# Optimization experiments

Hardware: AMD Instinct MI355X
Metric: run time of the kernel (lower is better)

Reference implementation:

```python
import jax, jax.numpy as jnp
import numpy as np

B, T, D, H = 4, 2048, 1024, 16
DH = D // H          # 64
HALF = DH // 2       # 32


def _rope_tables(T, half, base=10000.0):
    inv_freq = 1.0 / (base ** (np.arange(half, dtype=np.float32) / half))
    t = np.arange(T, dtype=np.float32)
    ang = np.outer(t, inv_freq)                       # [T, half]
    cos = jnp.asarray(np.cos(ang))[None, None]        # [1,1,T,half]
    sin = jnp.asarray(np.sin(ang))[None, None]
    return cos, sin


def setup_inputs() -> dict:
    key = jax.random.key(0)
    kx, kq, kp = jax.random.split(key, 3)
    cos, sin = _rope_tables(T, HALF)
    return {
        "x": jax.random.normal(kx, (B, T, D), dtype=jnp.float32),
        "cos": cos,
        "sin": sin,
        "W_qkv": jax.random.normal(kq, (3 * D, D), dtype=jnp.float32) * (D ** -0.5),
        "W_proj": jax.random.normal(kp, (D, D), dtype=jnp.float32) * (D ** -0.5),
    }


def _apply_rope(q, k, cos, sin):
    # q,k: [B,H,T,dh]; cos,sin: [1,1,T,dh/2]
    t = q.shape[2]
    c, s = cos[:, :, :t, :], sin[:, :, :t, :]
    h = q.shape[-1] // 2
    q1, q2 = q[..., :h], q[..., h:]
    k1, k2 = k[..., :h], k[..., h:]
    q_rot = jnp.concatenate([q1 * c - q2 * s, q1 * s + q2 * c], axis=-1)
    k_rot = jnp.concatenate([k1 * c - k2 * s, k1 * s + k2 * c], axis=-1)
    return q_rot, k_rot


def reference(x, cos, sin, W_qkv, W_proj):
    Bb, Tt, C = x.shape
    qkv = x @ W_qkv.T                                 # [B,T,3C]
    q, k, v = jnp.split(qkv, 3, axis=2)
    # [B,T,C] -> [B,H,T,dh]
    q = q.reshape(Bb, Tt, H, DH).transpose(0, 2, 1, 3)
    k = k.reshape(Bb, Tt, H, DH).transpose(0, 2, 1, 3)
    v = v.reshape(Bb, Tt, H, DH).transpose(0, 2, 1, 3)
    q, k = _apply_rope(q, k, cos, sin)
    w = jnp.einsum("bhqd,bhkd->bhqk", q, k) * (DH ** -0.5)
    causal = jnp.tril(jnp.ones((Tt, Tt), dtype=bool))
    w = jnp.where(causal, w, -jnp.inf)
    w = jax.nn.softmax(w.astype(jnp.float32), axis=-1).astype(x.dtype)
    out = jnp.einsum("bhqk,bhkd->bhqd", w, v)
    # XSA: subtract self-value contribution (diagonal attention weight)
    self_w = jnp.diagonal(w, axis1=-2, axis2=-1)[..., None]  # [B,H,T,1]
    out = out - self_w * v
    out = out.transpose(0, 2, 1, 3).reshape(Bb, Tt, C)
    return out @ W_proj.T
```

## Files before the change

kernel.cpp:

```cpp
#include <hip/hip_runtime.h>

constexpr int Tq = 2048;
constexpr int Dq = 1024;

typedef __bf16 bf16x8 __attribute__((ext_vector_type(8)));
typedef float f32x4 __attribute__((ext_vector_type(4)));
typedef _Float16 f16;
typedef f16 f16x4 __attribute__((ext_vector_type(4)));
typedef unsigned short u16;
typedef u16 u16x4 __attribute__((ext_vector_type(4)));
typedef u16 u16x8 __attribute__((ext_vector_type(8)));

__device__ __forceinline__ u16 f2bf(float f) {
    unsigned int u = __float_as_uint(f);
    u += 0x7fffu + ((u >> 16) & 1u);
    return (u16)(u >> 16);
}

__device__ __forceinline__ void gld_lds16(const void* g, void* l) {
    __builtin_amdgcn_global_load_lds(
        (const __attribute__((address_space(1))) unsigned int*)g,
        (__attribute__((address_space(3))) unsigned int*)l, 16, 0, 0);
}

__global__ void cvt3_f32_bf16(const float* __restrict__ a, u16* __restrict__ oa, int na,
                              const float* __restrict__ b, u16* __restrict__ ob, int nb,
                              const float* __restrict__ c, u16* __restrict__ oc, int nc) {
    int i = blockIdx.x * 256 + threadIdx.x;
    const float* in; u16* out;
    if (i < na) { in = a; out = oa; }
    else if (i < na + nb) { in = b; out = ob; i -= na; }
    else if (i < na + nb + nc) { in = c; out = oc; i -= na + nb; }
    else return;
    float4 v = ((const float4*)in)[i];
    u16x4 o;
    o.x = f2bf(v.x); o.y = f2bf(v.y); o.z = f2bf(v.z); o.w = f2bf(v.w);
    ((u16x4*)out)[i] = o;
}

__global__ __launch_bounds__(512, 2) void gemm_qkv(const u16* __restrict__ A,
                                                   const u16* __restrict__ B,
                                                   const float* __restrict__ cosT,
                                                   const float* __restrict__ sinT,
                                                   u16* __restrict__ Qb,
                                                   u16* __restrict__ Kb,
                                                   f16* __restrict__ Vtg) {
    constexpr int K = 1024, nk = K / 64;
    __shared__ __align__(16) u16 smem[65536];
    const int t = threadIdx.x;
    const int lane = t & 63;
    const int wave = t >> 6;
    const int l16 = lane & 15;
    const int quad = lane >> 4;
    const int wr = wave >> 2;
    const int wc = wave & 3;
    const int bm = blockIdx.x * 256;
    const int by = blockIdx.y;
    const int bn = by * 256;

    const int srow = t >> 3;
    const int sgc = (t & 7) ^ (srow & 7);
    const u16* Ab = A + (size_t)(bm + srow) * K + sgc * 8;
    const u16* Bb = B + (size_t)(bn + srow) * K + sgc * 8;

    f32x4 acc[8][4] = {};

    auto stageA = [&](int kt, int q) {
        gld_lds16(Ab + (size_t)q * 64 * K + kt * 64,
                  (char*)smem + (kt & 1) * 65536 + q * 8192 + t * 16);
    };
    auto stageB = [&](int kt, int q) {
        gld_lds16(Bb + (size_t)q * 64 * K + kt * 64,
                  (char*)smem + (kt & 1) * 65536 + 32768 + q * 8192 + t * 16);
    };

    stageB(0, 0); stageB(0, 1); stageB(0, 2); stageB(0, 3);
    stageA(0, 0); stageA(0, 2); stageA(0, 1); stageA(0, 3);

    const int cc0 = quad ^ (l16 & 7);
    const int cc1 = (4 + quad) ^ (l16 & 7);

    for (int kt = 0; kt < nk; kt++) {
        const u16* As = smem + (kt & 1) * 32768;
        const u16* Bs = As + 16384;
        const bool pre = (kt + 1 < nk);

        asm volatile("s_waitcnt vmcnt(2)\n\ts_barrier" ::: "memory");

        bf16x8 af[4], bf[4];
        if (pre) { stageB(kt + 1, 0); stageB(kt + 1, 1); }
#pragma unroll
        for (int m = 0; m < 4; m++)
            af[m] = *(const bf16x8*)&As[(wr * 128 + m * 16 + l16) * 64 + cc0 * 8];
#pragma unroll
        for (int n = 0; n < 4; n++)
            bf[n] = *(const bf16x8*)&Bs[(wc * 64 + n * 16 + l16) * 64 + cc0 * 8];
        __builtin_amdgcn_s_setprio(1);
#pragma unroll
        for (int m = 0; m < 4; m++)
#pragma unroll
            for (int n = 0; n < 4; n++)
                acc[m][n] = __builtin_amdgcn_mfma_f32_16x16x32_bf16(af[m], bf[n], acc[m][n], 0, 0, 0);
        __builtin_amdgcn_s_setprio(0);

        if (pre) asm volatile("s_waitcnt vmcnt(2)\n\ts_barrier" ::: "memory");
        else     asm volatile("s_waitcnt vmcnt(0)\n\ts_barrier" ::: "memory");

        if (pre) { stageB(kt + 1, 2); stageB(kt + 1, 3); }
#pragma unroll
        for (int m = 0; m < 4; m++)
            af[m] = *(const bf16x8*)&As[(wr * 128 + (m + 4) * 16 + l16) * 64 + cc0 * 8];
        __builtin_amdgcn_s_setprio(1);
#pragma unroll
        for (int m = 0; m < 4; m++)
#pragma unroll
            for (int n = 0; n < 4; n++)
                acc[m + 4][n] = __builtin_amdgcn_mfma_f32_16x16x32_bf16(af[m], bf[n], acc[m + 4][n], 0, 0, 0);
        __builtin_amdgcn_s_setprio(0);

        if (pre) { stageA(kt + 1, 0); stageA(kt + 1, 2); }
#pragma unroll
        for (int m = 0; m < 4; m++)
            af[m] = *(const bf16x8*)&As[(wr * 128 + m * 16 + l16) * 64 + cc1 * 8];
#pragma unroll
        for (int n = 0; n < 4; n++)
            bf[n] = *(const bf16x8*)&Bs[(wc * 64 + n * 16 + l16) * 64 + cc1 * 8];
        __builtin_amdgcn_s_setprio(1);
#pragma unroll
        for (int m = 0; m < 4; m++)
#pragma unroll
            for (int n = 0; n < 4; n++)
                acc[m][n] = __builtin_amdgcn_mfma_f32_16x16x32_bf16(af[m], bf[n], acc[m][n], 0, 0, 0);
        __builtin_amdgcn_s_setprio(0);

        if (pre) { stageA(kt + 1, 1); stageA(kt + 1, 3); }
#pragma unroll
        for (int m = 0; m < 4; m++)
            af[m] = *(const bf16x8*)&As[(wr * 128 + (m + 4) * 16 + l16) * 64 + cc1 * 8];
        __builtin_amdgcn_s_setprio(1);
#pragma unroll
        for (int m = 0; m < 4; m++)
#pragma unroll
            for (int n = 0; n < 4; n++)
                acc[m + 4][n] = __builtin_amdgcn_mfma_f32_16x16x32_bf16(af[m], bf[n], acc[m + 4][n], 0, 0, 0);
        __builtin_amdgcn_s_setprio(0);
    }

    const int kind = by >> 2;
    if (kind < 2) {
        u16* Out = kind ? Kb : Qb;
        const float qscale = kind ? 1.f : 0.18033688011112042f;
        const int h = ((by & 3) << 2) + wc;
#pragma unroll
        for (int m = 0; m < 8; m++)
#pragma unroll
            for (int r = 0; r < 4; r++) {
                const int gm = bm + wr * 128 + m * 16 + quad * 4 + r;
                const int b = gm >> 11, tt = gm & 2047;
                const size_t row = ((size_t)(b * 16 + h) * Tq + tt) * 64;
#pragma unroll
                for (int jj = 0; jj < 2; jj++) {
                    const int dd = jj * 16 + l16;
                    const float c = cosT[tt * 32 + dd];
                    const float s = sinT[tt * 32 + dd];
                    const float v1 = acc[m][jj][r];
                    const float v2 = acc[m][jj + 2][r];
                    Out[row + dd]      = f2bf((v1 * c - v2 * s) * qscale);
                    Out[row + dd + 32] = f2bf((v1 * s + v2 * c) * qscale);
                }
            }
    } else {
        const int h = ((by & 3) << 2) + wc;
#pragma unroll
        for (int m = 0; m < 8; m++) {
            const int gm0 = bm + wr * 128 + m * 16 + quad * 4;
            const int b = gm0 >> 11, tt = gm0 & 2047;
#pragma unroll
            for (int n = 0; n < 4; n++) {
                const int d = n * 16 + l16;
                f16x4 o = {(f16)acc[m][n][0], (f16)acc[m][n][1],
                           (f16)acc[m][n][2], (f16)acc[m][n][3]};
                *(f16x4*)&Vtg[((size_t)(b * 16 + h) * 64 + d) * Tq + tt] = o;
            }
        }
    }
}

__global__ __launch_bounds__(256) void gemm_bt(const u16* __restrict__ A,
                                               const u16* __restrict__ B,
                                               float* __restrict__ Cv,
                                               int M, int N, int K) {
    __shared__ u16 As[128 * 32];
    __shared__ u16 Bs[128 * 32];
    const int t = threadIdx.x;
    const int lane = t & 63;
    const int wave = t >> 6;
    const int l16 = lane & 15;
    const int quad = lane >> 4;
    const int bm = blockIdx.x * 128;
    const int bn = blockIdx.y * 128;
    const int wm = (wave & 1) * 64;
    const int wn = (wave >> 1) * 64;
    const int srow = t >> 2;
    const int scol = (t & 3) * 8;

    f32x4 acc[4][4] = {};

    const u16* Ab = A + (size_t)(bm + srow) * K + scol;
    const u16* Bb = B + (size_t)(bn + srow) * K + scol;

    for (int k0 = 0; k0 < K; k0 += 32) {
        gld_lds16(Ab + k0,                    (char*)As + t * 16);
        gld_lds16(Ab + (size_t)64 * K + k0,   (char*)As + 4096 + t * 16);
        gld_lds16(Bb + k0,                    (char*)Bs + t * 16);
        gld_lds16(Bb + (size_t)64 * K + k0,   (char*)Bs + 4096 + t * 16);
        __syncthreads();

        bf16x8 af[4], bf[4];
#pragma unroll
        for (int i = 0; i < 4; i++) {
            af[i] = *(const bf16x8*)&As[(wm + i * 16 + l16) * 32 + quad * 8];
            bf[i] = *(const bf16x8*)&Bs[(wn + i * 16 + l16) * 32 + quad * 8];
        }
#pragma unroll
        for (int i = 0; i < 4; i++)
#pragma unroll
            for (int j = 0; j < 4; j++)
                acc[i][j] = __builtin_amdgcn_mfma_f32_16x16x32_bf16(af[i], bf[j], acc[i][j], 0, 0, 0);
        __syncthreads();
    }

#pragma unroll
    for (int i = 0; i < 4; i++)
#pragma unroll
        for (int j = 0; j < 4; j++)
#pragma unroll
            for (int r = 0; r < 4; r++) {
                const int gm = bm + wm + i * 16 + quad * 4 + r;
                const int gn = bn + wn + j * 16 + l16;
                Cv[(size_t)gm * N + gn] = acc[i][j][r];
            }
}

template <bool MASK>
__device__ __forceinline__ void flash_tile(const u16* __restrict__ Ks,
                                           const f16* __restrict__ Vs,
                                           const bf16x8& qf0, const bf16x8& qf1,
                                           int l16, int quad, int i_loc,
                                           float& l_run, f32x4* o_acc) {
    f32x4 s[4];
    const int cp0 = quad ^ (l16 & 7);
    const int cp1 = (4 + quad) ^ (l16 & 7);
    __builtin_amdgcn_s_setprio(1);
#pragma unroll
    for (int tn = 0; tn < 4; tn++) {
        const int jrow = tn * 16 + l16;
        bf16x8 kf0 = *(const bf16x8*)&Ks[jrow * 64 + cp0 * 8];
        bf16x8 kf1 = *(const bf16x8*)&Ks[jrow * 64 + cp1 * 8];
        f32x4 z = {0.f, 0.f, 0.f, 0.f};
        z = __builtin_amdgcn_mfma_f32_16x16x32_bf16(kf0, qf0, z, 0, 0, 0);
        z = __builtin_amdgcn_mfma_f32_16x16x32_bf16(kf1, qf1, z, 0, 0, 0);
        s[tn] = z;
    }
    __builtin_amdgcn_s_setprio(0);
    float rsa[4];
#pragma unroll
    for (int tn = 0; tn < 4; tn++) {
        float rs = 0.f;
#pragma unroll
        for (int r = 0; r < 4; r++) {
            float v = s[tn][r];
            if (MASK) {
                const int j_loc = tn * 16 + quad * 4 + r;
                if (j_loc > i_loc) v = -1e30f;
            }
            float p = exp2f(v);
            rs += p;
            if (MASK) {
                const int j_loc = tn * 16 + quad * 4 + r;
                if (j_loc == i_loc) p = 0.f;
            }
            s[tn][r] = p;
        }
        rsa[tn] = rs;
    }
    l_run += (rsa[0] + rsa[1]) + (rsa[2] + rsa[3]);

    f16x4 pf[4];
#pragma unroll
    for (int tk = 0; tk < 4; tk++)
        pf[tk] = f16x4{(f16)s[tk][0], (f16)s[tk][1], (f16)s[tk][2], (f16)s[tk][3]};
    __builtin_amdgcn_s_setprio(1);
#pragma unroll
    for (int td = 0; td < 4; td++) {
        const int drow = td * 16 + l16;
#pragma unroll
        for (int tk = 0; tk < 4; tk++) {
            const int cp = (2 * tk + (quad >> 1)) ^ (l16 & 7);
            f16x4 vf = *(const f16x4*)&Vs[drow * 64 + cp * 8 + (quad & 1) * 4];
            o_acc[td] = __builtin_amdgcn_mfma_f32_16x16x16f16(vf, pf[tk], o_acc[td], 0, 0, 0);
        }
    }
    __builtin_amdgcn_s_setprio(0);
}

__global__ __launch_bounds__(512, 4) void flash(const u16* __restrict__ Qb,
                                                const u16* __restrict__ Kb,
                                                const f16* __restrict__ Vtg,
                                                u16* __restrict__ Ob) {
    __shared__ __align__(16) char smem[65536];

    const int t = threadIdx.x, lane = t & 63, wave = t >> 6;
    const int l16 = lane & 15, quad = lane >> 4;
    const int i = blockIdx.x;
    const int xcd = i & 7, w = i >> 3;
    const int bh = xcd * 8 + (w >> 4);
    const int b = bh >> 4, h = bh & 15;
    const int x = w & 15;
    const int qt = (wave < 4) ? x : (31 - x);
    const int q0w = qt * 64;
    const u16* Qp = Qb + (size_t)bh * Tq * 64;
    const u16* Kp = Kb + (size_t)bh * Tq * 64;
    const f16* Vp = Vtg + (size_t)bh * 64 * Tq;

    const int i_abs = q0w + (wave & 3) * 16 + l16;
    bf16x8 qf0 = *(const bf16x8*)(Qp + (size_t)i_abs * 64 + quad * 8);
    bf16x8 qf1 = *(const bf16x8*)(Qp + (size_t)i_abs * 64 + 32 + quad * 8);
    asm volatile("s_waitcnt vmcnt(0)" : "+v"(qf0), "+v"(qf1) :: "memory");

    float l_run = 0.f;
    f32x4 o_acc[4] = {};

    const int srow = t >> 3;
    const int sc = (t & 7) ^ (srow & 7);
    const int diag_n = qt;
    const int i_tloc = (wave & 3) * 16 + l16;
    const int nt = 32 - x;

    auto stage = [&](int n) {
        const int j0 = n * 64;
        char* buf = smem + (n & 3) * 16384;
        gld_lds16(Kp + (size_t)(j0 + srow) * 64 + sc * 8, buf + t * 16);
        gld_lds16(Vp + (size_t)srow * Tq + j0 + sc * 8,   buf + 8192 + t * 16);
    };

    stage(0);
    stage(1);
    for (int n = 0; n < nt; n++) {
        char* cur = smem + (n & 3) * 16384;
        if (n + 2 < nt) {
            stage(n + 2);
            asm volatile("s_waitcnt vmcnt(4)\n\ts_barrier" ::: "memory");
        } else if (n + 1 < nt) {
            asm volatile("s_waitcnt vmcnt(2)\n\ts_barrier" ::: "memory");
        } else {
            asm volatile("s_waitcnt vmcnt(0)\n\ts_barrier" ::: "memory");
        }
        const u16* Ks = (const u16*)cur;
        const f16* Vs = (const f16*)(cur + 8192);
        if (n < diag_n)
            flash_tile<false>(Ks, Vs, qf0, qf1, l16, quad, i_tloc, l_run, o_acc);
        else if (n == diag_n)
            flash_tile<true>(Ks, Vs, qf0, qf1, l16, quad, i_tloc, l_run, o_acc);
    }

    l_run += __shfl_xor(l_run, 16, 64);
    l_run += __shfl_xor(l_run, 32, 64);
    const float inv_l = 1.f / l_run;

    __syncthreads();
    u16* Os = (u16*)smem;
#pragma unroll
    for (int td = 0; td < 4; td++) {
        u16x4 o;
#pragma unroll
        for (int r = 0; r < 4; r++) o[r] = f2bf(o_acc[td][r] * inv_l);
        *(u16x4*)&Os[wave * 1152 + l16 * 72 + td * 16 + quad * 4] = o;
    }
    __syncthreads();
    const int oi = lane >> 2, od = (lane & 3) * 16;
    u16x8 r0 = *(const u16x8*)&Os[wave * 1152 + oi * 72 + od];
    u16x8 r1 = *(const u16x8*)&Os[wave * 1152 + oi * 72 + od + 8];
    const size_t orow = ((size_t)b * Tq + q0w + (wave & 3) * 16 + oi) * Dq + h * 64 + od;
    *(u16x8*)&Ob[orow] = r0;
    *(u16x8*)&Ob[orow + 8] = r1;
}

extern "C" void kernel_launch(void* const* d_in, const int* in_sizes, int n_in,
                              void* d_out, int out_size, void* d_ws, size_t ws_size,
                              hipStream_t stream) {
    const float* x     = (const float*)d_in[0];
    const float* cosT  = (const float*)d_in[1];
    const float* sinT  = (const float*)d_in[2];
    const float* Wqkv  = (const float*)d_in[3];
    const float* Wproj = (const float*)d_in[4];

    u16* xb     = (u16*)d_ws;
    u16* wqkvb  = xb + (size_t)8192 * 1024;
    u16* wprojb = wqkvb + (size_t)3072 * 1024;
    u16* Qb     = wprojb + (size_t)1024 * 1024;
    u16* Kb     = Qb + (size_t)64 * 2048 * 64;
    f16* Vtg    = (f16*)(Kb + (size_t)64 * 2048 * 64);
    u16* attn   = (u16*)(Vtg + (size_t)64 * 64 * 2048);

    cvt3_f32_bf16<<<12288, 256, 0, stream>>>(x, xb, 2097152,
                                             Wqkv, wqkvb, 786432,
                                             Wproj, wprojb, 262144);

    gemm_qkv<<<dim3(32, 12), 512, 0, stream>>>(xb, wqkvb, cosT, sinT, Qb, Kb, Vtg);
    flash<<<1024, 512, 0, stream>>>(Qb, Kb, Vtg, attn);
    gemm_bt<<<dim3(64, 8), 256, 0, stream>>>(attn, wprojb, (float*)d_out, 8192, 1024, 1024);
}
```

Before: 267.4 us.

## Simplify QKV GEMM to 128x128 single-buffered tiles and double flash K/V staging

Replaces the 256x256 double-buffered, software-pipelined QKV GEMM with a simple 128x128-tile kernel. That kernel loads K-slices of 32 directly to LDS and synchronises twice per iteration, with no prefetch overlap or swizzle. The flash kernel now stages two 64-key tiles per step into a two-slot buffer and waits with vmcnt(0), replacing the 3-deep single-tile ring. This trades latency hiding and data reuse for more blocks and simpler code. It also risks LDS bank conflicts from the removed XOR swizzle in the GEMM.

```diff
diff --git a/kernel.cpp b/kernel.cpp
--- a/kernel.cpp
+++ b/kernel.cpp
@@ -38,124 +38,65 @@
     ((u16x4*)out)[i] = o;
 }
 
-__global__ __launch_bounds__(512, 2) void gemm_qkv(const u16* __restrict__ A,
-                                                   const u16* __restrict__ B,
-                                                   const float* __restrict__ cosT,
-                                                   const float* __restrict__ sinT,
-                                                   u16* __restrict__ Qb,
-                                                   u16* __restrict__ Kb,
-                                                   f16* __restrict__ Vtg) {
-    constexpr int K = 1024, nk = K / 64;
-    __shared__ __align__(16) u16 smem[65536];
+__global__ __launch_bounds__(256) void gemm_qkv(const u16* __restrict__ A,
+                                                const u16* __restrict__ B,
+                                                const float* __restrict__ cosT,
+                                                const float* __restrict__ sinT,
+                                                u16* __restrict__ Qb,
+                                                u16* __restrict__ Kb,
+                                                f16* __restrict__ Vtg) {
+    constexpr int K = 1024, N = 3072;
+    __shared__ u16 As[128 * 32];
+    __shared__ u16 Bs[128 * 32];
     const int t = threadIdx.x;
     const int lane = t & 63;
     const int wave = t >> 6;
     const int l16 = lane & 15;
     const int quad = lane >> 4;
-    const int wr = wave >> 2;
-    const int wc = wave & 3;
-    const int bm = blockIdx.x * 256;
+    const int bm = blockIdx.x * 128;
     const int by = blockIdx.y;
-    const int bn = by * 256;
-
-    const int srow = t >> 3;
-    const int sgc = (t & 7) ^ (srow & 7);
-    const u16* Ab = A + (size_t)(bm + srow) * K + sgc * 8;
-    const u16* Bb = B + (size_t)(bn + srow) * K + sgc * 8;
-
-    f32x4 acc[8][4] = {};
-
-    auto stageA = [&](int kt, int q) {
-        gld_lds16(Ab + (size_t)q * 64 * K + kt * 64,
-                  (char*)smem + (kt & 1) * 65536 + q * 8192 + t * 16);
-    };
-    auto stageB = [&](int kt, int q) {
-        gld_lds16(Bb + (size_t)q * 64 * K + kt * 64,
-                  (char*)smem + (kt & 1) * 65536 + 32768 + q * 8192 + t * 16);
-    };
-
-    stageB(0, 0); stageB(0, 1); stageB(0, 2); stageB(0, 3);
-    stageA(0, 0); stageA(0, 2); stageA(0, 1); stageA(0, 3);
-
-    const int cc0 = quad ^ (l16 & 7);
-    const int cc1 = (4 + quad) ^ (l16 & 7);
-
-    for (int kt = 0; kt < nk; kt++) {
-        const u16* As = smem + (kt & 1) * 32768;
-        const u16* Bs = As + 16384;
-        const bool pre = (kt + 1 < nk);
-
-        asm volatile("s_waitcnt vmcnt(2)\n\ts_barrier" ::: "memory");
+    const int bn = by * 128;
+    const int wm = (wave & 1) * 64;
+    const int wn = (wave >> 1) * 64;
+    const int srow = t >> 2;
+    const int scol = (t & 3) * 8;
+
+    f32x4 acc[4][4] = {};
+
+    const u16* Ab = A + (size_t)(bm + srow) * K + scol;
+    const u16* Bb = B + (size_t)(bn + srow) * K + scol;
+
+    for (int k0 = 0; k0 < K; k0 += 32) {
+        gld_lds16(Ab + k0,                    (char*)As + t * 16);
+        gld_lds16(Ab + (size_t)64 * K + k0,   (char*)As + 4096 + t * 16);
+        gld_lds16(Bb + k0,                    (char*)Bs + t * 16);
+        gld_lds16(Bb + (size_t)64 * K + k0,   (char*)Bs + 4096 + t * 16);
+        __syncthreads();
 
         bf16x8 af[4], bf[4];
-        if (pre) { stageB(kt + 1, 0); stageB(kt + 1, 1); }
-#pragma unroll
-        for (int m = 0; m < 4; m++)
-            af[m] = *(const bf16x8*)&As[(wr * 128 + m * 16 + l16) * 64 + cc0 * 8];
-#pragma unroll
-        for (int n = 0; n < 4; n++)
-            bf[n] = *(const bf16x8*)&Bs[(wc * 64 + n * 16 + l16) * 64 + cc0 * 8];
-        __builtin_amdgcn_s_setprio(1);
-#pragma unroll
-        for (int m = 0; m < 4; m++)
-#pragma unroll
-            for (int n = 0; n < 4; n++)
-                acc[m][n] = __builtin_amdgcn_mfma_f32_16x16x32_bf16(af[m], bf[n], acc[m][n], 0, 0, 0);
-        __builtin_amdgcn_s_setprio(0);
-
-        if (pre) asm volatile("s_waitcnt vmcnt(2)\n\ts_barrier" ::: "memory");
-        else     asm volatile("s_waitcnt vmcnt(0)\n\ts_barrier" ::: "memory");
-
-        if (pre) { stageB(kt + 1, 2); stageB(kt + 1, 3); }
-#pragma unroll
-        for (int m = 0; m < 4; m++)
-            af[m] = *(const bf16x8*)&As[(wr * 128 + (m + 4) * 16 + l16) * 64 + cc0 * 8];
-        __builtin_amdgcn_s_setprio(1);
-#pragma unroll
-        for (int m = 0; m < 4; m++)
-#pragma unroll
-            for (int n = 0; n < 4; n++)
-                acc[m + 4][n] = __builtin_amdgcn_mfma_f32_16x16x32_bf16(af[m], bf[n], acc[m + 4][n], 0, 0, 0);
-        __builtin_amdgcn_s_setprio(0);
-
-        if (pre) { stageA(kt + 1, 0); stageA(kt + 1, 2); }
-#pragma unroll
-        for (int m = 0; m < 4; m++)
-            af[m] = *(const bf16x8*)&As[(wr * 128 + m * 16 + l16) * 64 + cc1 * 8];
-#pragma unroll
-        for (int n = 0; n < 4; n++)
-            bf[n] = *(const bf16x8*)&Bs[(wc * 64 + n * 16 + l16) * 64 + cc1 * 8];
-        __builtin_amdgcn_s_setprio(1);
-#pragma unroll
-        for (int m = 0; m < 4; m++)
-#pragma unroll
-            for (int n = 0; n < 4; n++)
-                acc[m][n] = __builtin_amdgcn_mfma_f32_16x16x32_bf16(af[m], bf[n], acc[m][n], 0, 0, 0);
-        __builtin_amdgcn_s_setprio(0);
-
-        if (pre) { stageA(kt + 1, 1); stageA(kt + 1, 3); }
-#pragma unroll
-        for (int m = 0; m < 4; m++)
-            af[m] = *(const bf16x8*)&As[(wr * 128 + (m + 4) * 16 + l16) * 64 + cc1 * 8];
-        __builtin_amdgcn_s_setprio(1);
-#pragma unroll
-        for (int m = 0; m < 4; m++)
-#pragma unroll
-            for (int n = 0; n < 4; n++)
-                acc[m + 4][n] = __builtin_amdgcn_mfma_f32_16x16x32_bf16(af[m], bf[n], acc[m + 4][n], 0, 0, 0);
-        __builtin_amdgcn_s_setprio(0);
-    }
-
-    const int kind = by >> 2;
+#pragma unroll
+        for (int i = 0; i < 4; i++) {
+            af[i] = *(const bf16x8*)&As[(wm + i * 16 + l16) * 32 + quad * 8];
+            bf[i] = *(const bf16x8*)&Bs[(wn + i * 16 + l16) * 32 + quad * 8];
+        }
+#pragma unroll
+        for (int i = 0; i < 4; i++)
+#pragma unroll
+            for (int j = 0; j < 4; j++)
+                acc[i][j] = __builtin_amdgcn_mfma_f32_16x16x32_bf16(af[i], bf[j], acc[i][j], 0, 0, 0);
+        __syncthreads();
+    }
+
+    const int kind = by >> 3;
     if (kind < 2) {
         u16* Out = kind ? Kb : Qb;
         const float qscale = kind ? 1.f : 0.18033688011112042f;
-        const int h = ((by & 3) << 2) + wc;
-#pragma unroll
-        for (int m = 0; m < 8; m++)
+        const int h = ((by & 7) << 1) + (wn >> 6);
+#pragma unroll
+        for (int i = 0; i < 4; i++)
 #pragma unroll
             for (int r = 0; r < 4; r++) {
-                const int gm = bm + wr * 128 + m * 16 + quad * 4 + r;
+                const int gm = bm + wm + i * 16 + quad * 4 + r;
                 const int b = gm >> 11, tt = gm & 2047;
                 const size_t row = ((size_t)(b * 16 + h) * Tq + tt) * 64;
 #pragma unroll
@@ -163,23 +104,24 @@
                     const int dd = jj * 16 + l16;
                     const float c = cosT[tt * 32 + dd];
                     const float s = sinT[tt * 32 + dd];
-                    const float v1 = acc[m][jj][r];
-                    const float v2 = acc[m][jj + 2][r];
+                    const float v1 = acc[i][jj][r];
+                    const float v2 = acc[i][jj + 2][r];
                     Out[row + dd]      = f2bf((v1 * c - v2 * s) * qscale);
                     Out[row + dd + 32] = f2bf((v1 * s + v2 * c) * qscale);
                 }
             }
     } else {
-        const int h = ((by & 3) << 2) + wc;
-#pragma unroll
-        for (int m = 0; m < 8; m++) {
-            const int gm0 = bm + wr * 128 + m * 16 + quad * 4;
+#pragma unroll
+        for (int i = 0; i < 4; i++) {
+            const int gm0 = bm + wm + i * 16 + quad * 4;
             const int b = gm0 >> 11, tt = gm0 & 2047;
 #pragma unroll
-            for (int n = 0; n < 4; n++) {
-                const int d = n * 16 + l16;
-                f16x4 o = {(f16)acc[m][n][0], (f16)acc[m][n][1],
-                           (f16)acc[m][n][2], (f16)acc[m][n][3]};
+            for (int j = 0; j < 4; j++) {
+                const int col = wn + j * 16 + l16;
+                const int h = ((by & 7) << 1) + (col >> 6);
+                const int d = col & 63;
+                f16x4 o = {(f16)acc[i][j][0], (f16)acc[i][j][1],
+                           (f16)acc[i][j][2], (f16)acc[i][j][3]};
                 *(f16x4*)&Vtg[((size_t)(b * 16 + h) * 64 + d) * Tq + tt] = o;
             }
         }
@@ -336,32 +278,32 @@
     const int diag_n = qt;
     const int i_tloc = (wave & 3) * 16 + l16;
     const int nt = 32 - x;
-
-    auto stage = [&](int n) {
-        const int j0 = n * 64;
-        char* buf = smem + (n & 3) * 16384;
-        gld_lds16(Kp + (size_t)(j0 + srow) * 64 + sc * 8, buf + t * 16);
-        gld_lds16(Vp + (size_t)srow * Tq + j0 + sc * 8,   buf + 8192 + t * 16);
+    const int nt2 = (nt + 1) >> 1;
+
+    auto stage = [&](int n2) {
+        const int j0 = n2 * 128;
+        char* buf = smem + (n2 & 1) * 32768;
+        gld_lds16(Kp + (size_t)(j0 + srow) * 64 + sc * 8,      buf + t * 16);
+        gld_lds16(Kp + (size_t)(j0 + 64 + srow) * 64 + sc * 8, buf + 8192 + t * 16);
+        gld_lds16(Vp + (size_t)srow * Tq + j0 + sc * 8,        buf + 16384 + t * 16);
+        gld_lds16(Vp + (size_t)srow * Tq + j0 + 64 + sc * 8,   buf + 24576 + t * 16);
     };
 
     stage(0);
-    stage(1);
-    for (int n = 0; n < nt; n++) {
-        char* cur = smem + (n & 3) * 16384;
-        if (n + 2 < nt) {
-            stage(n + 2);
-            asm volatile("s_waitcnt vmcnt(4)\n\ts_barrier" ::: "memory");
-        } else if (n + 1 < nt) {
-            asm volatile("s_waitcnt vmcnt(2)\n\ts_barrier" ::: "memory");
-        } else {
-            asm volatile("s_waitcnt vmcnt(0)\n\ts_barrier" ::: "memory");
-        }
-        const u16* Ks = (const u16*)cur;
-        const f16* Vs = (const f16*)(cur + 8192);
-        if (n < diag_n)
-            flash_tile<false>(Ks, Vs, qf0, qf1, l16, quad, i_tloc, l_run, o_acc);
-        else if (n == diag_n)
-            flash_tile<true>(Ks, Vs, qf0, qf1, l16, quad, i_tloc, l_run, o_acc);
+    for (int n2 = 0; n2 < nt2; n2++) {
+        asm volatile("s_waitcnt vmcnt(0)\n\ts_barrier" ::: "memory");
+        if (n2 + 1 < nt2) stage(n2 + 1);
+        char* cb = smem + (n2 & 1) * 32768;
+#pragma unroll
+        for (int s = 0; s < 2; s++) {
+            const int tile = n2 * 2 + s;
+            const u16* Ks = (const u16*)(cb + s * 8192);
+            const f16* Vs = (const f16*)(cb + 16384 + s * 8192);
+            if (tile < diag_n)
+                flash_tile<false>(Ks, Vs, qf0, qf1, l16, quad, i_tloc, l_run, o_acc);
+            else if (tile == diag_n)
+                flash_tile<true>(Ks, Vs, qf0, qf1, l16, quad, i_tloc, l_run, o_acc);
+        }
     }
 
     l_run += __shfl_xor(l_run, 16, 64);
@@ -407,7 +349,7 @@
                                              Wqkv, wqkvb, 786432,
                                              Wproj, wprojb, 262144);
 
-    gemm_qkv<<<dim3(32, 12), 512, 0, stream>>>(xb, wqkvb, cosT, sinT, Qb, Kb, Vtg);
+    gemm_qkv<<<dim3(64, 24), 256, 0, stream>>>(xb, wqkvb, cosT, sinT, Qb, Kb, Vtg);
     flash<<<1024, 512, 0, stream>>>(Qb, Kb, Vtg, attn);
     gemm_bt<<<dim3(64, 8), 256, 0, stream>>>(attn, wprojb, (float*)d_out, 8192, 1024, 1024);
 }
```

Result: no change. 263.0 us (-1.6%).
